# Optimization experiments

Measured on AMD Instinct MI355X. Metric: run time of the kernel, lower is better.

## Reference

```python
import jax, jax.numpy as jnp
import numpy as np

N = 4096          # num nodes
D = 128           # feature dim (dataset.x.shape[-1])
E = 131072        # num edges (avg degree 32)
POOL_K = 0.6      # ks[0]
K = max(2, int(POOL_K * N))  # 2457 kept nodes


def setup_inputs() -> dict:
    key = jax.random.key(0)
    ks = jax.random.split(key, 8)
    s = 0.05
    g = jax.random.randint(ks[0], (2, E), 0, N)                      # edge_index
    h = jax.random.normal(ks[1], (N, D), jnp.float32)                # node features
    Wd = jax.random.normal(ks[2], (D, D), jnp.float32) * s           # down-GCN stub
    bd = jnp.zeros((D,), jnp.float32)
    pw = jax.random.normal(ks[3], (D, 1), jnp.float32) * s           # Pool.proj weight
    pb = jnp.zeros((1,), jnp.float32)                                # Pool.proj bias
    Wb = jax.random.normal(ks[4], (D, D), jnp.float32) * s           # bottom-GCN stub
    bb = jnp.zeros((D,), jnp.float32)
    Wu = jax.random.normal(ks[5], (D, D), jnp.float32) * s           # up-GCN stub
    bu = jnp.zeros((D,), jnp.float32)
    return {"g": g, "h": h, "Wd": Wd, "bd": bd, "pw": pw, "pb": pb,
            "Wb": Wb, "bb": bb, "Wu": Wu, "bu": bu}


def reference(g, h, Wd, bd, pw, pb, Wb, bb, Wu, bu):
    dt = h.dtype
    src, dst = g[0], g[1]
    # to_dense_adj: scatter-add edges into dense [N, N] adjacency
    adj = jnp.zeros((N, N), dt).at[src, dst].add(jnp.ones((E,), dt))

    # down GCN (GNNEarly stub, called with h only): linear
    h0 = h @ Wd + bd

    # Pool: score, topk, gather
    scores = jax.nn.sigmoid((h0 @ pw + pb)[:, 0])          # [N]
    values, idx = jax.lax.top_k(scores, K)                 # descending, like torch.topk
    new_h = h0[idx] * values[:, None]                      # [K, D]

    # boolean 2-hop connectivity, then subselect pooled nodes
    un_g = (adj > 0).astype(dt)
    two_hop = ((un_g @ un_g) > 0).astype(dt)               # [N, N]
    sub = two_hop[idx][:, idx]                             # [K, K]
    # norm_g: g / degrees with torch broadcasting => column-normalize by row-degree
    degrees = jnp.sum(sub, axis=1)                         # [K]
    g_p = sub / degrees                                    # sub[i,j] / degrees[j]

    # bottom GCN (stub with pooled graph): propagate + linear
    h_b = g_p @ (new_h @ Wb) + bb                          # [K, D]

    # Unpool: scatter back to N nodes
    h_u = jnp.zeros((N, D), dt).at[idx].set(h_b)

    # up GCN (stub with original dense adj adj_ms[0])
    h_up = adj @ (h_u @ Wu) + bu                           # [N, D]

    h1 = h_up + h0        # h.add(down_outs[0])
    h2 = h1 + h           # h.add(org_h)
    return (h1, h2)       # hs list
```

## Files before the change

### kernel.cpp

```cpp
#include <hip/hip_runtime.h>
#include <hip/hip_bf16.h>
#include <stdint.h>


#define NN 4096
#define DD 128
#define KKEEP 2457
#define SUBW 40
#define MP 2464
#define KP 2560
#define MT 154
#define NT 8
#define KCHUNK (KP / 4)
#define RT 8

typedef unsigned long long u64;
typedef unsigned short ushort_t;
typedef __attribute__((ext_vector_type(8))) short bf16x8;
typedef __attribute__((ext_vector_type(4))) float f32x4;

__global__ void k_zero(float4* __restrict__ p) {
    int i = blockIdx.x * 256 + threadIdx.x;
    p[i] = make_float4(0.f, 0.f, 0.f, 0.f);
}

__global__ void k_h0_build(const float* __restrict__ h, const float* __restrict__ Wd,
                           const float* __restrict__ bd, const float* __restrict__ pw,
                           const float* __restrict__ pb, const int* __restrict__ g, int E,
                           float* __restrict__ h0, float* __restrict__ scores,
                           u64* __restrict__ rowbits, int* __restrict__ deg) {
    __shared__ float rows[RT][DD];
    __shared__ float sred[2][RT];
    int bid = blockIdx.x;
    int d = threadIdx.x;
    if (bid >= NN / RT) {
        int e = (bid - NN / RT) * 128 + d;
        if (e < E) {
            int s = g[e], d2 = g[E + e];
            atomicOr(&rowbits[(size_t)s * 64 + (d2 >> 6)], 1ull << (d2 & 63));
            atomicAdd(&deg[s], 1);
        }
        return;
    }
    int r0 = bid * RT;
    #pragma unroll
    for (int r = 0; r < RT; ++r) rows[r][d] = h[(size_t)(r0 + r) * DD + d];
    __syncthreads();
    float acc[RT];
    float b = bd[d];
    #pragma unroll
    for (int r = 0; r < RT; ++r) acc[r] = b;
    for (int kb = 0; kb < DD; kb += 16) {
        float w[16];
        #pragma unroll
        for (int j = 0; j < 16; ++j) w[j] = Wd[(size_t)(kb + j) * DD + d];
        #pragma unroll
        for (int r = 0; r < RT; ++r)
            #pragma unroll
            for (int j = 0; j < 16; ++j) acc[r] += rows[r][kb + j] * w[j];
    }
    #pragma unroll
    for (int r = 0; r < RT; ++r) h0[(size_t)(r0 + r) * DD + d] = acc[r];
    float pwd = pw[d];
    int lane = d & 63, wv = d >> 6;
    #pragma unroll
    for (int r = 0; r < RT; ++r) {
        float v = acc[r] * pwd;
        #pragma unroll
        for (int s = 32; s > 0; s >>= 1) v += __shfl_xor(v, s);
        if (lane == 0) sred[wv][r] = v;
    }
    __syncthreads();
    if (d < RT) {
        float v = sred[0][d] + sred[1][d];
        scores[r0 + d] = 1.0f / (1.0f + expf(-(v + pb[0])));
    }
}

__global__ void k_rank_scan(const float* __restrict__ scores, const int* __restrict__ deg,
                            int* __restrict__ keep, int* __restrict__ pos,
                            int* __restrict__ idxl, int* __restrict__ off) {
    int bid = blockIdx.x;
    int t = threadIdx.x;
    if (bid == NN / 4) {
        __shared__ int part[256];
        int base = t * 16;
        int loc[16]; int s = 0;
        #pragma unroll
        for (int i = 0; i < 16; ++i) { loc[i] = s; s += deg[base + i]; }
        part[t] = s;
        __syncthreads();
        int sum = 0;
        for (int i = 0; i < t; ++i) sum += part[i];
        #pragma unroll
        for (int i = 0; i < 16; ++i) off[base + i] = sum + loc[i];
        if (t == 255) off[NN] = sum + s;
        return;
    }
    int lane = t & 63;
    int i = bid * 4 + (t >> 6);
    float my = scores[i];
    int rank = 0;
    #pragma unroll 4
    for (int base = 0; base < NN; base += 64) {
        int jj = base + lane;
        float sj = scores[jj];
        u64 m = __ballot((sj > my) || (sj == my && jj < i));
        rank += __popcll(m);
    }
    if (lane == 0) {
        if (rank < KKEEP) { keep[i] = 1; pos[i] = rank; idxl[rank] = i; }
        else keep[i] = 0;
    }
}

__global__ void k_sub_scatter(const u64* __restrict__ rowbits, const int* __restrict__ idxl,
                              const int* __restrict__ g, int E, const int* __restrict__ off,
                              const int* __restrict__ keep, const int* __restrict__ pos,
                              int* __restrict__ cursor, int* __restrict__ csrv,
                              ushort_t* __restrict__ S, float* __restrict__ invdeg) {
    __shared__ int nb[320];
    __shared__ int nbcnt;
    __shared__ int cntS;
    __shared__ u64 accLDS[64];
    int bid = blockIdx.x;
    int t = threadIdx.x;
    if (bid >= MP) {
        int e = (bid - MP) * 256 + t;
        if (e < E) {
            int s = g[e], dd = g[E + e];
            int p = atomicAdd(&cursor[s], 1);
            csrv[off[s] + p] = keep[dd] ? pos[dd] : -1;
        }
        return;
    }
    int r = bid;
    int wv = t >> 6, lane = t & 63;
    ushort_t* Srow = S + (size_t)r * KP;
    if (r >= KKEEP) {
        #pragma unroll
        for (int j = 0; j < 10; ++j) Srow[j * 256 + t] = 0;
        return;
    }
    int i = idxl[r];
    if (wv == 0) {
        u64 rw = rowbits[(size_t)i * 64 + lane];
        int myc = __popcll(rw);
        int pre = myc;
        #pragma unroll
        for (int s = 1; s < 64; s <<= 1) {
            int tt = __shfl_up(pre, s);
            if (lane >= s) pre += tt;
        }
        pre -= myc;
        u64 w = rw; int j = 0;
        while (w) {
            int b = __builtin_ctzll(w);
            w &= w - 1;
            nb[pre + j] = lane * 64 + b; ++j;
        }
        if (lane == 63) nbcnt = pre + myc;
    } else if (wv == 1) {
        accLDS[lane] = 0;
    } else if (wv == 2 && lane == 0) {
        cntS = 0;
    }
    __syncthreads();
    int cnt_nb = nbcnt;
    u64 accw = 0;
    for (int j = wv; j < cnt_nb; j += 4)
        accw |= rowbits[(size_t)nb[j] * 64 + lane];
    atomicOr(&accLDS[lane], accw);
    __syncthreads();
    int cntp = 0;
    #pragma unroll
    for (int wjj = 0; wjj < 10; ++wjj) {
        int wj = wv * 10 + wjj;
        int c = wj * 64 + lane;
        int ci = (c < KKEEP) ? idxl[c] : 0;
        u64 w = accLDS[ci >> 6];
        int bit = (c < KKEEP) ? (int)((w >> (ci & 63)) & 1ull) : 0;
        cntp += __popcll(__ballot(bit));
        Srow[c] = bit ? 0x3F80 : 0;
    }
    if (lane == 0) atomicAdd(&cntS, cntp);
    __syncthreads();
    if (t == 0) invdeg[r] = 1.0f / (float)cntS;
}

__global__ void k_t(const float* __restrict__ h0, const float* __restrict__ scores,
                    const int* __restrict__ idxl, const float* __restrict__ Wb,
                    const float* __restrict__ invdeg, ushort_t* __restrict__ tT) {
    __shared__ float rows[RT][DD];
    int d = threadIdx.x;
    int r0 = blockIdx.x * RT;
    #pragma unroll
    for (int r = 0; r < RT; ++r) {
        int rr = r0 + r;
        float v = 0.f;
        if (rr < KKEEP) {
            int i = idxl[rr];
            v = h0[(size_t)i * DD + d] * scores[i];
        }
        rows[r][d] = v;
    }
    __syncthreads();
    float acc[RT];
    #pragma unroll
    for (int r = 0; r < RT; ++r) acc[r] = 0.f;
    for (int kb = 0; kb < DD; kb += 16) {
        float w[16];
        #pragma unroll
        for (int j = 0; j < 16; ++j) w[j] = Wb[(size_t)(kb + j) * DD + d];
        #pragma unroll
        for (int r = 0; r < RT; ++r)
            #pragma unroll
            for (int j = 0; j < 16; ++j) acc[r] += rows[r][kb + j] * w[j];
    }
    bf16x8 packed;
    #pragma unroll
    for (int r = 0; r < RT; ++r) {
        int rr = r0 + r;
        float v = (rr < KKEEP) ? acc[r] * invdeg[rr] : 0.f;
        __hip_bfloat16 b = __float2bfloat16(v);
        packed[r] = *reinterpret_cast<short*>(&b);
    }
    *reinterpret_cast<bf16x8*>(tT + (size_t)d * KP + r0) = packed;
}

__global__ void k_gemm(const short* __restrict__ S, const short* __restrict__ tT,
                       float* __restrict__ hb) {
    __shared__ f32x4 red[4][64];
    int tile = blockIdx.x;
    int wv = threadIdx.x >> 6, lane = threadIdx.x & 63;
    int rt = tile >> 3, ct = tile & 7;
    const short* arow = S + (size_t)(rt * 16 + (lane & 15)) * KP + ((lane >> 4) * 8) + wv * KCHUNK;
    const short* brow = tT + (size_t)(ct * 16 + (lane & 15)) * KP + ((lane >> 4) * 8) + wv * KCHUNK;
    f32x4 acc = {0.f, 0.f, 0.f, 0.f};
    #pragma unroll 4
    for (int kk = 0; kk < KCHUNK; kk += 32) {
        bf16x8 a = *(const bf16x8*)(arow + kk);
        bf16x8 b = *(const bf16x8*)(brow + kk);
        acc = __builtin_amdgcn_mfma_f32_16x16x32_bf16(a, b, acc, 0, 0, 0);
    }
    red[wv][lane] = acc;
    __syncthreads();
    if (wv == 0) {
        f32x4 s = red[0][lane] + red[1][lane] + red[2][lane] + red[3][lane];
        int col = ct * 16 + (lane & 15);
        int row0 = rt * 16 + ((lane >> 4) * 4);
        #pragma unroll
        for (int j = 0; j < 4; ++j) {
            int row = row0 + j;
            if (row < KKEEP) hb[(size_t)row * DD + col] = s[j];
        }
    }
}

__global__ void k_u(const float* __restrict__ hb, const float* __restrict__ bb,
                    const float* __restrict__ Wu, float* __restrict__ uu) {
    __shared__ float rows[RT][DD];
    int d = threadIdx.x;
    int r0 = blockIdx.x * RT;
    float bias = bb[d];
    #pragma unroll
    for (int r = 0; r < RT; ++r) {
        int rr = r0 + r;
        rows[r][d] = (rr < KKEEP) ? hb[(size_t)rr * DD + d] + bias : 0.f;
    }
    __syncthreads();
    float acc[RT];
    #pragma unroll
    for (int r = 0; r < RT; ++r) acc[r] = 0.f;
    for (int kb = 0; kb < DD; kb += 16) {
        float w[16];
        #pragma unroll
        for (int j = 0; j < 16; ++j) w[j] = Wu[(size_t)(kb + j) * DD + d];
        #pragma unroll
        for (int r = 0; r < RT; ++r)
            #pragma unroll
            for (int j = 0; j < 16; ++j) acc[r] += rows[r][kb + j] * w[j];
    }
    #pragma unroll
    for (int r = 0; r < RT; ++r) {
        int rr = r0 + r;
        if (rr < KKEEP) uu[(size_t)rr * DD + d] = acc[r];
    }
}

__global__ void k_agg(const int* __restrict__ off, const int* __restrict__ csrv,
                      const float* __restrict__ uu, const float* __restrict__ bu,
                      const float* __restrict__ h0, const float* __restrict__ h,
                      float* __restrict__ out) {
    int s = blockIdx.x, d = threadIdx.x;
    int b = off[s], e2 = off[s + 1];
    float acc = 0.f;
    int k = b;
    for (; k + 4 <= e2; k += 4) {
        int v0 = csrv[k], v1 = csrv[k + 1], v2 = csrv[k + 2], v3 = csrv[k + 3];
        float a0 = (v0 >= 0) ? uu[(size_t)v0 * DD + d] : 0.f;
        float a1 = (v1 >= 0) ? uu[(size_t)v1 * DD + d] : 0.f;
        float a2 = (v2 >= 0) ? uu[(size_t)v2 * DD + d] : 0.f;
        float a3 = (v3 >= 0) ? uu[(size_t)v3 * DD + d] : 0.f;
        acc += (a0 + a1) + (a2 + a3);
    }
    for (; k < e2; ++k) {
        int v = csrv[k];
        if (v >= 0) acc += uu[(size_t)v * DD + d];
    }
    size_t o = (size_t)s * DD + d;
    float a = acc + bu[d] + h0[o];
    out[o] = a;
    out[(size_t)NN * DD + o] = a + h[o];
}

extern "C" void kernel_launch(void* const* d_in, const int* in_sizes, int n_in,
                              void* d_out, int out_size, void* d_ws, size_t ws_size,
                              hipStream_t stream) {
    const int*   g  = (const int*)d_in[0];
    const float* h  = (const float*)d_in[1];
    const float* Wd = (const float*)d_in[2];
    const float* bd = (const float*)d_in[3];
    const float* pw = (const float*)d_in[4];
    const float* pb = (const float*)d_in[5];
    const float* Wb = (const float*)d_in[6];
    const float* bb = (const float*)d_in[7];
    const float* Wu = (const float*)d_in[8];
    const float* bu = (const float*)d_in[9];
    float* out = (float*)d_out;
    const int E = in_sizes[0] / 2;

    char* ws = (char*)d_ws;
    ushort_t* S       = (ushort_t*)(ws + 0);
    float*    uu      = (float*)(ws + 0);
    u64*      rowbits = (u64*)  (ws + (13u << 20));
    int*      deg     = (int*)  (ws + (15u << 20));
    int*      cursor  = (int*)  (ws + (15u << 20) + 16384);
    int*      off     = (int*)  (ws + (15u << 20) + 32768);
    float*    h0      = (float*)(ws + (16u << 20));
    ushort_t* tT      = (ushort_t*)(ws + (18u << 20));
    float*    hb      = (float*)(ws + (19u << 20));
    int*      csrv    = (int*)  (ws + (21u << 20));
    float*    scores  = (float*)(ws + (22u << 20));
    float*    invdeg  = (float*)(ws + (22u << 20) + 16384);
    int*      pos     = (int*)  (ws + (22u << 20) + 32768);
    int*      keep    = (int*)  (ws + (22u << 20) + 49152);
    int*      idxl    = (int*)  (ws + (22u << 20) + 65536);

    k_zero<<<520, 256, 0, stream>>>((float4*)rowbits);

    k_h0_build<<<NN / RT + E / 128, 128, 0, stream>>>(h, Wd, bd, pw, pb, g, E,
                                                      h0, scores, rowbits, deg);
    k_rank_scan<<<NN / 4 + 1, 256, 0, stream>>>(scores, deg, keep, pos, idxl, off);
    k_sub_scatter<<<MP + E / 256, 256, 0, stream>>>(rowbits, idxl, g, E, off,
                                                    keep, pos, cursor, csrv, S, invdeg);
    k_t<<<KP / RT, DD, 0, stream>>>(h0, scores, idxl, Wb, invdeg, tT);
    k_gemm<<<MT * NT, 256, 0, stream>>>((const short*)S, (const short*)tT, hb);
    k_u<<<(KKEEP + RT - 1) / RT, DD, 0, stream>>>(hb, bb, Wu, uu);
    k_agg<<<NN, DD, 0, stream>>>(off, csrv, uu, bu, h0, h, out);
}
```

Measured before the change: 123.8 us.

## Fold Wb·Wu into one precomputed weight and drop the k_u kernel

Uses associativity, (g_p·(new_h·Wb) + bb)·Wu = g_p·(new_h·(Wb·Wu)) + bb·Wu, to precompute W2 = Wb·Wu and cu = bb·Wu inside extra blocks of the first kernel. The projection kernel then uses W2, and the MFMA gemm writes uu directly with cu added, so the separate k_u launch and the hb round trip go away. This changes the rounding, since the combined product passes through bf16 once. It also adds 17 serial blocks to the first kernel, with a naive 128-step loop for cu.

```diff
diff --git a/kernel.cpp b/kernel.cpp
--- a/kernel.cpp
+++ b/kernel.cpp
@@ -27,14 +27,45 @@
 __global__ void k_h0_build(const float* __restrict__ h, const float* __restrict__ Wd,
                            const float* __restrict__ bd, const float* __restrict__ pw,
                            const float* __restrict__ pb, const int* __restrict__ g, int E,
+                           const float* __restrict__ Wb, const float* __restrict__ Wu,
+                           const float* __restrict__ bb,
                            float* __restrict__ h0, float* __restrict__ scores,
-                           u64* __restrict__ rowbits, int* __restrict__ deg) {
+                           u64* __restrict__ rowbits, int* __restrict__ deg,
+                           float* __restrict__ W2, float* __restrict__ cu) {
     __shared__ float rows[RT][DD];
     __shared__ float sred[2][RT];
     int bid = blockIdx.x;
     int d = threadIdx.x;
-    if (bid >= NN / RT) {
-        int e = (bid - NN / RT) * 128 + d;
+    if (bid >= 1536) {
+        int wb = bid - 1536;
+        if (wb < 16) {
+            int r0 = wb * RT;
+            #pragma unroll
+            for (int r = 0; r < RT; ++r) rows[r][d] = Wb[(size_t)(r0 + r) * DD + d];
+            __syncthreads();
+            float acc[RT];
+            #pragma unroll
+            for (int r = 0; r < RT; ++r) acc[r] = 0.f;
+            for (int kb = 0; kb < DD; kb += 16) {
+                float w[16];
+                #pragma unroll
+                for (int j = 0; j < 16; ++j) w[j] = Wu[(size_t)(kb + j) * DD + d];
+                #pragma unroll
+                for (int r = 0; r < RT; ++r)
+                    #pragma unroll
+                    for (int j = 0; j < 16; ++j) acc[r] += rows[r][kb + j] * w[j];
+            }
+            #pragma unroll
+            for (int r = 0; r < RT; ++r) W2[(size_t)(r0 + r) * DD + d] = acc[r];
+        } else {
+            float a = 0.f;
+            for (int m = 0; m < DD; ++m) a += bb[m] * Wu[(size_t)m * DD + d];
+            cu[d] = a;
+        }
+        return;
+    }
+    if (bid >= 512) {
+        int e = (bid - 512) * 128 + d;
         if (e < E) {
             int s = g[e], d2 = g[E + e];
             atomicOr(&rowbits[(size_t)s * 64 + (d2 >> 6)], 1ull << (d2 & 63));
@@ -148,9 +179,9 @@
         int myc = __popcll(rw);
         int pre = myc;
         #pragma unroll
-        for (int s = 1; s < 64; s <<= 1) {
-            int tt = __shfl_up(pre, s);
-            if (lane >= s) pre += tt;
+        for (int s2 = 1; s2 < 64; s2 <<= 1) {
+            int tt = __shfl_up(pre, s2);
+            if (lane >= s2) pre += tt;
         }
         pre -= myc;
         u64 w = rw; int j = 0;
@@ -188,9 +219,9 @@
     if (t == 0) invdeg[r] = 1.0f / (float)cntS;
 }
 
-__global__ void k_t(const float* __restrict__ h0, const float* __restrict__ scores,
-                    const int* __restrict__ idxl, const float* __restrict__ Wb,
-                    const float* __restrict__ invdeg, ushort_t* __restrict__ tT) {
+__global__ void k_t2(const float* __restrict__ h0, const float* __restrict__ scores,
+                     const int* __restrict__ idxl, const float* __restrict__ W2,
+                     const float* __restrict__ invdeg, ushort_t* __restrict__ tT) {
     __shared__ float rows[RT][DD];
     int d = threadIdx.x;
     int r0 = blockIdx.x * RT;
@@ -211,7 +242,7 @@
     for (int kb = 0; kb < DD; kb += 16) {
         float w[16];
         #pragma unroll
-        for (int j = 0; j < 16; ++j) w[j] = Wb[(size_t)(kb + j) * DD + d];
+        for (int j = 0; j < 16; ++j) w[j] = W2[(size_t)(kb + j) * DD + d];
         #pragma unroll
         for (int r = 0; r < RT; ++r)
             #pragma unroll
@@ -229,7 +260,7 @@
 }
 
 __global__ void k_gemm(const short* __restrict__ S, const short* __restrict__ tT,
-                       float* __restrict__ hb) {
+                       const float* __restrict__ cu, float* __restrict__ uu) {
     __shared__ f32x4 red[4][64];
     int tile = blockIdx.x;
     int wv = threadIdx.x >> 6, lane = threadIdx.x & 63;
@@ -248,43 +279,13 @@
     if (wv == 0) {
         f32x4 s = red[0][lane] + red[1][lane] + red[2][lane] + red[3][lane];
         int col = ct * 16 + (lane & 15);
+        float cuv = cu[col];
         int row0 = rt * 16 + ((lane >> 4) * 4);
         #pragma unroll
         for (int j = 0; j < 4; ++j) {
             int row = row0 + j;
-            if (row < KKEEP) hb[(size_t)row * DD + col] = s[j];
-        }
-    }
-}
-
-__global__ void k_u(const float* __restrict__ hb, const float* __restrict__ bb,
-                    const float* __restrict__ Wu, float* __restrict__ uu) {
-    __shared__ float rows[RT][DD];
-    int d = threadIdx.x;
-    int r0 = blockIdx.x * RT;
-    float bias = bb[d];
-    #pragma unroll
-    for (int r = 0; r < RT; ++r) {
-        int rr = r0 + r;
-        rows[r][d] = (rr < KKEEP) ? hb[(size_t)rr * DD + d] + bias : 0.f;
-    }
-    __syncthreads();
-    float acc[RT];
-    #pragma unroll
-    for (int r = 0; r < RT; ++r) acc[r] = 0.f;
-    for (int kb = 0; kb < DD; kb += 16) {
-        float w[16];
-        #pragma unroll
-        for (int j = 0; j < 16; ++j) w[j] = Wu[(size_t)(kb + j) * DD + d];
-        #pragma unroll
-        for (int r = 0; r < RT; ++r)
-            #pragma unroll
-            for (int j = 0; j < 16; ++j) acc[r] += rows[r][kb + j] * w[j];
-    }
-    #pragma unroll
-    for (int r = 0; r < RT; ++r) {
-        int rr = r0 + r;
-        if (rr < KKEEP) uu[(size_t)rr * DD + d] = acc[r];
+            if (row < KKEEP) uu[(size_t)row * DD + col] = s[j] + cuv;
+        }
     }
 }
 
@@ -328,34 +329,33 @@
     const float* Wu = (const float*)d_in[8];
     const float* bu = (const float*)d_in[9];
     float* out = (float*)d_out;
-    const int E = in_sizes[0] / 2;
+    int E = in_sizes[0] / 2;
 
     char* ws = (char*)d_ws;
     ushort_t* S       = (ushort_t*)(ws + 0);
-    float*    uu      = (float*)(ws + 0);
     u64*      rowbits = (u64*)  (ws + (13u << 20));
     int*      deg     = (int*)  (ws + (15u << 20));
     int*      cursor  = (int*)  (ws + (15u << 20) + 16384);
     int*      off     = (int*)  (ws + (15u << 20) + 32768);
     float*    h0      = (float*)(ws + (16u << 20));
     ushort_t* tT      = (ushort_t*)(ws + (18u << 20));
-    float*    hb      = (float*)(ws + (19u << 20));
     int*      csrv    = (int*)  (ws + (21u << 20));
-    float*    scores  = (float*)(ws + (22u << 20));
-    float*    invdeg  = (float*)(ws + (22u << 20) + 16384);
-    int*      pos     = (int*)  (ws + (22u << 20) + 32768);
-    int*      keep    = (int*)  (ws + (22u << 20) + 49152);
-    int*      idxl    = (int*)  (ws + (22u << 20) + 65536);
+    float*    uu      = (float*)(ws + (22u << 20));
+    float*    scores  = (float*)(ws + (24u << 20));
+    float*    invdeg  = (float*)(ws + (24u << 20) + 16384);
+    int*      pos     = (int*)  (ws + (24u << 20) + 32768);
+    int*      keep    = (int*)  (ws + (24u << 20) + 49152);
+    int*      idxl    = (int*)  (ws + (24u << 20) + 65536);
+    float*    W2      = (float*)(ws + (24u << 20) + 98304);
+    float*    cu      = (float*)(ws + (24u << 20) + 98304 + 65536);
 
     k_zero<<<520, 256, 0, stream>>>((float4*)rowbits);
-
-    k_h0_build<<<NN / RT + E / 128, 128, 0, stream>>>(h, Wd, bd, pw, pb, g, E,
-                                                      h0, scores, rowbits, deg);
+    k_h0_build<<<1553, 128, 0, stream>>>(h, Wd, bd, pw, pb, g, E, Wb, Wu, bb,
+                                         h0, scores, rowbits, deg, W2, cu);
     k_rank_scan<<<NN / 4 + 1, 256, 0, stream>>>(scores, deg, keep, pos, idxl, off);
     k_sub_scatter<<<MP + E / 256, 256, 0, stream>>>(rowbits, idxl, g, E, off,
                                                     keep, pos, cursor, csrv, S, invdeg);
-    k_t<<<KP / RT, DD, 0, stream>>>(h0, scores, idxl, Wb, invdeg, tT);
-    k_gemm<<<MT * NT, 256, 0, stream>>>((const short*)S, (const short*)tT, hb);
-    k_u<<<(KKEEP + RT - 1) / RT, DD, 0, stream>>>(hb, bb, Wu, uu);
+    k_t2<<<KP / RT, DD, 0, stream>>>(h0, scores, idxl, W2, invdeg, tT);
+    k_gemm<<<MT * NT, 256, 0, stream>>>((const short*)S, (const short*)tT, cu, uu);
     k_agg<<<NN, DD, 0, stream>>>(off, csrv, uu, bu, h0, h, out);
 }
```

After: 113.2 us. -8.6%, faster.
